# Kernel optimization log

Hardware: AMD Instinct MI355X
Metric: run time of the kernel (lower is better)

Reference implementation:

```python
import jax, jax.numpy as jnp
import numpy as np

B, S, D, H = 4, 2048, 1024, 16
DK = D // H
THETA = 10000.0


def setup_inputs() -> dict:
    key = jax.random.key(0)
    ks = jax.random.split(key, 5)
    std = (1.0 / D) ** 0.5
    return {
        "x": jax.random.normal(ks[0], (B, S, D), dtype=jnp.float32),
        "q_proj": jax.random.normal(ks[1], (D, D), dtype=jnp.float32) * std,
        "k_proj": jax.random.normal(ks[2], (D, D), dtype=jnp.float32) * std,
        "v_proj": jax.random.normal(ks[3], (D, D), dtype=jnp.float32) * std,
        "o_proj": jax.random.normal(ks[4], (D, D), dtype=jnp.float32) * std,
        "token_positions": jnp.broadcast_to(jnp.arange(S, dtype=jnp.int32), (B, S)),
    }


def _apply_rope(t, cos, sin):
    # t: (B,H,S,DK); cos/sin: (B,1,S,DK//2). Interleaved even/odd rotation.
    even = t[..., 0::2]
    odd = t[..., 1::2]
    r_even = even * cos - odd * sin
    r_odd = even * sin + odd * cos
    return jnp.stack([r_even, r_odd], axis=-1).reshape(t.shape)


def reference(x, q_proj, k_proj, v_proj, o_proj, token_positions):
    b, s, d = x.shape
    # QKV projections: weights stored (out, in) -> x @ W^T
    q = (x @ q_proj.T).reshape(b, s, H, DK).transpose(0, 2, 1, 3)  # (B,H,S,DK)
    k = (x @ k_proj.T).reshape(b, s, H, DK).transpose(0, 2, 1, 3)
    v = (x @ v_proj.T).reshape(b, s, H, DK).transpose(0, 2, 1, 3)

    # RoPE angles from token positions
    inv_freq = 1.0 / (THETA ** (jnp.arange(0, DK, 2, dtype=jnp.float32) / DK))  # (DK/2,)
    ang = token_positions.astype(jnp.float32)[..., None] * inv_freq  # (B,S,DK/2)
    cos = jnp.cos(ang)[:, None, :, :]  # (B,1,S,DK/2)
    sin = jnp.sin(ang)[:, None, :, :]
    q = _apply_rope(q, cos, sin)
    k = _apply_rope(k, cos, sin)

    # Full causal attention with explicit score matrix (faithful to source)
    scores = jnp.einsum("bhqd,bhkd->bhqk", q, k) / (DK ** 0.5)
    causal = jnp.tril(jnp.ones((s, s), dtype=bool))
    scores = jnp.where(causal, scores, -jnp.inf)
    attn = jax.nn.softmax(scores, axis=-1)
    out = jnp.einsum("bhqk,bhkd->bhqd", attn, v)  # (B,H,S,DK)
    out = out.transpose(0, 2, 1, 3).reshape(b, s, d)  # (B,S,D)
    # o_proj stored (d_out, d_model): out @ o_proj^T
    return out @ o_proj.T
```

## Files before the change

### kernel.cpp

```cpp
#include <hip/hip_runtime.h>
#include <hip/hip_bf16.h>

using bf16x8 = __attribute__((ext_vector_type(8))) short;
using f32x4  = __attribute__((ext_vector_type(4))) float;

#define MFMA_BF16(a, b, c) __builtin_amdgcn_mfma_f32_16x16x32_bf16((a), (b), (c), 0, 0, 0)

__device__ __forceinline__ unsigned short f2bf(float x) {
  union { float f; unsigned int u; } v; v.f = x;
  unsigned int r = v.u + 0x7fffu + ((v.u >> 16) & 1u);
  return (unsigned short)(r >> 16);
}

__device__ __forceinline__ unsigned int cvtpk(float a, float b) {
  __hip_bfloat162 h = __float22bfloat162_rn(make_float2(a, b));
  unsigned int u; __builtin_memcpy(&u, &h, 4); return u;
}

__device__ __forceinline__ unsigned int pack_trunc(float a, float b) {
  unsigned int ua, ub;
  __builtin_memcpy(&ua, &a, 4);
  __builtin_memcpy(&ub, &b, 4);
  return (ua >> 16) | (ub & 0xFFFF0000u);
}

__device__ __forceinline__ float fast_exp2(float x) {
#if __has_builtin(__builtin_amdgcn_exp2f)
  return __builtin_amdgcn_exp2f(x);
#else
  return exp2f(x);
#endif
}

__device__ __forceinline__ void gload16(const void* g, void* l) {
  __builtin_amdgcn_global_load_lds(
      (const __attribute__((address_space(1))) unsigned int*)g,
      (__attribute__((address_space(3))) unsigned int*)l, 16, 0, 0);
}

__device__ __forceinline__ void wait_and_barrier() {
  asm volatile("s_waitcnt vmcnt(0)" ::: "memory");
  __builtin_amdgcn_sched_barrier(0);
  __builtin_amdgcn_s_barrier();
  __builtin_amdgcn_sched_barrier(0);
}

__global__ __launch_bounds__(256) void cvt_all(const float* __restrict__ x,
                                               const float* __restrict__ qw,
                                               const float* __restrict__ kw,
                                               const float* __restrict__ vw,
                                               const float* __restrict__ ow,
                                               unsigned short* __restrict__ out) {
  const int bid = blockIdx.x;
  int seg, loc;
  if (bid < 8192) { seg = 0; loc = bid; }
  else { seg = 1 + ((bid - 8192) >> 10); loc = (bid - 8192) & 1023; }
  const float* srcs[5] = {x, qw, kw, vw, ow};
  const float* in = srcs[seg];
  const size_t obase = (seg == 0) ? 0 : ((size_t)8192 + (size_t)(seg - 1) * 1024) * 1024;
  const int i = loc * 1024 + threadIdx.x * 4;
  float4 f = *(const float4*)(in + i);
  ushort4 o;
  o.x = f2bf(f.x); o.y = f2bf(f.y); o.z = f2bf(f.z); o.w = f2bf(f.w);
  *(ushort4*)(out + obase + i) = o;
}

__global__ __launch_bounds__(256) void rope_tab_k(const int* __restrict__ pos,
                                                  float2* __restrict__ tab) {
  const int row = blockIdx.x * 8 + (threadIdx.x >> 5);
  const int i = threadIdx.x & 31;
  const float p = (float)pos[row];
  const float invf = exp2f((float)(2 * i) * (-13.287712379549609f / 64.0f));
  float sn, cs;
  sincosf(p * invf, &sn, &cs);
  tab[(size_t)row * 32 + i] = make_float2(cs, sn);
}

template <int MODE>
__global__ __launch_bounds__(256) void gemm_bt(const unsigned short* __restrict__ A,
                                               const unsigned short* __restrict__ Bw,
                                               void* __restrict__ outp,
                                               const float2* __restrict__ tab,
                                               float oscale) {
  constexpr int K = 1024;
  __shared__ __align__(16) unsigned short smem[12288];
  const int tid  = threadIdx.x;
  const int lane = tid & 63, wave = tid >> 6;
  const int wr = wave >> 1, wc = wave & 1;
  const int bid = blockIdx.x + (blockIdx.y << 3);
  const int xcd = bid & 7;
  const int t6  = bid >> 3;
  const int bn0 = (t6 & 7) * 128;
  const int bm0 = (((t6 >> 3) << 3) + xcd) * 64;
  const int lrow = lane & 15, hi = lane >> 4, lko = hi * 8;
  const int srow = tid >> 2, scol = (tid & 3) * 8;
  const unsigned short* gA = A + (size_t)(bm0 + srow) * K + scol;
  const unsigned short* gB = Bw + (size_t)(bn0 + srow) * K + scol;
  const f32x4 z = {0.f, 0.f, 0.f, 0.f};
  f32x4 acc[2][4];
#pragma unroll
  for (int i = 0; i < 2; ++i)
#pragma unroll
    for (int j = 0; j < 4; ++j) acc[i][j] = z;

  auto stage = [&](int k0, int c) {
    char* base = (char*)smem + c * 12288;
    gload16(gA + k0, base + wave * 1024);
    gload16(gB + k0, base + 4096 + wave * 1024);
    gload16(gB + k0 + (size_t)64 * K, base + 8192 + wave * 1024);
  };

  stage(0, 0);
  int cur = 0;
#pragma unroll 1
  for (int k0 = 0; k0 < K; k0 += 32) {
    wait_and_barrier();
    if (k0 + 32 < K) stage(k0 + 32, cur ^ 1);
    const int ub = cur * 6144;
    bf16x8 af[2], bfr[4];
#pragma unroll
    for (int mi = 0; mi < 2; ++mi)
      af[mi] = *(const bf16x8*)&smem[ub + (wr * 32 + mi * 16 + lrow) * 32 + lko];
#pragma unroll
    for (int ni = 0; ni < 4; ++ni)
      bfr[ni] = *(const bf16x8*)&smem[ub + 2048 + (wc * 64 + ni * 16 + lrow) * 32 + lko];
#pragma unroll
    for (int mi = 0; mi < 2; ++mi)
#pragma unroll
      for (int ni = 0; ni < 4; ++ni)
        acc[mi][ni] = MFMA_BF16(af[mi], bfr[ni], acc[mi][ni]);
    cur ^= 1;
  }

  if (MODE == 2) {
#pragma unroll
    for (int mi = 0; mi < 2; ++mi)
#pragma unroll
      for (int r = 0; r < 4; ++r) {
        const int row = bm0 + wr * 32 + mi * 16 + hi * 4 + r;
#pragma unroll
        for (int ni = 0; ni < 4; ++ni) {
          const int col = bn0 + wc * 64 + ni * 16 + lrow;
          ((float*)outp)[(size_t)row * 1024 + col] = acc[mi][ni][r];
        }
      }
    return;
  }

  const int h0 = bn0 >> 6;
  const int bb = bm0 >> 11, s0 = bm0 & 2047;
  unsigned short* dst = (unsigned short*)outp;
  __syncthreads();
  if (MODE == 0) {
#pragma unroll
    for (int mi = 0; mi < 2; ++mi)
#pragma unroll
      for (int ni = 0; ni < 4; ++ni) {
        const int col = wc * 64 + ni * 16 + lrow;
        const int d = col & 63;
#pragma unroll
        for (int r = 0; r < 4; ++r) {
          const int row = wr * 32 + mi * 16 + hi * 4 + r;
          const float2 t = tab[(size_t)(bm0 + row) * 32 + (d >> 1)];
          const float v = acc[mi][ni][r];
          const float other = __shfl_xor(v, 1);
          const float rv = (d & 1) ? (other * t.y + v * t.x) : (v * t.x - other * t.y);
          smem[row * 136 + col] = f2bf(rv * oscale);
        }
      }
    __syncthreads();
#pragma unroll
    for (int it = 0; it < 4; ++it) {
      const int c = it * 256 + tid;
      const int hl = c >> 9, rem = c & 511;
      const int sl = rem >> 3, ch = (rem & 7) * 8;
      const bf16x8 val = *(const bf16x8*)&smem[sl * 136 + hl * 64 + ch];
      *(bf16x8*)&dst[((size_t)(bb * 16 + h0 + hl) * 2048 + s0 + sl) * 64 + ch] = val;
    }
  } else {
#pragma unroll
    for (int mi = 0; mi < 2; ++mi)
#pragma unroll
      for (int ni = 0; ni < 4; ++ni) {
        const int col = wc * 64 + ni * 16 + lrow;
        ushort4 pk;
        pk.x = f2bf(acc[mi][ni][0]); pk.y = f2bf(acc[mi][ni][1]);
        pk.z = f2bf(acc[mi][ni][2]); pk.w = f2bf(acc[mi][ni][3]);
        *(ushort4*)&smem[col * 72 + wr * 32 + mi * 16 + hi * 4] = pk;
      }
    __syncthreads();
#pragma unroll
    for (int it = 0; it < 4; ++it) {
      const int c = it * 256 + tid;
      const int cl = c >> 3, sc = (c & 7) * 8;
      const bf16x8 val = *(const bf16x8*)&smem[cl * 72 + sc];
      *(bf16x8*)&dst[((size_t)(bb * 16 + h0 + (cl >> 6)) * 64 + (cl & 63)) * 2048 + s0 + sc] = val;
    }
  }
}

__global__ __launch_bounds__(256) void attn_fwd(const unsigned short* __restrict__ Q,
                                                const unsigned short* __restrict__ Kk,
                                                const unsigned short* __restrict__ Vt,
                                                unsigned short* __restrict__ O) {
  __shared__ __align__(16) unsigned short Ks[4096];
  __shared__ __align__(16) unsigned short Vs[4096];
  __shared__ __align__(16) unsigned short Plds[4][16][64];
  const int p = blockIdx.x;
  const int L = (p & 7) * 128 + (p >> 3);
  const int bh = L >> 4, pair = L & 15;
  const int tid = threadIdx.x;
  const int lane = tid & 63, wave = tid >> 6;
  const int lrow = lane & 15, hi = lane >> 4;
  const int l7 = lrow & 7;
  const unsigned short* Qb = Q + (size_t)bh * 2048 * 64;
  const unsigned short* Kb = Kk + (size_t)bh * 2048 * 64;
  const unsigned short* Vb = Vt + (size_t)bh * 64 * 2048;
  const int rowA = tid >> 3;
  const int colA = ((tid & 7) ^ (rowA & 7)) * 8;
  const int rowB = rowA + 32;
  const int colB = ((tid & 7) ^ (rowB & 7)) * 8;
  char* kBase0 = (char*)Ks + wave * 1024;
  char* kBase1 = (char*)Ks + 4096 + wave * 1024;
  char* vBase0 = (char*)Vs + wave * 1024;
  char* vBase1 = (char*)Vs + 4096 + wave * 1024;
  const int b = bh >> 4, h = bh & 15;
  const f32x4 z = {0.f, 0.f, 0.f, 0.f};
  const short one = (short)0x3F80;
  const bf16x8 ones = {one, one, one, one, one, one, one, one};

  for (int half = 0; half < 2; ++half) {
    const int qb = half ? (31 - pair) : pair;
    const int qrow = qb * 64 + wave * 16;
    const int qg = qrow + lrow;
    const bf16x8 qf0 = *(const bf16x8*)(Qb + (size_t)qg * 64 + hi * 8);
    const bf16x8 qf1 = *(const bf16x8*)(Qb + (size_t)qg * 64 + 32 + hi * 8);
    f32x4 acc[4] = {z, z, z, z};
    f32x4 acc_l = z;

    auto process = [&](int t, bool diag) {
      const int kv0 = t * 64;
      __syncthreads();
      gload16(Kb + (size_t)(kv0 + rowA) * 64 + colA, kBase0);
      gload16(Kb + (size_t)(kv0 + rowB) * 64 + colB, kBase1);
      gload16(Vb + (size_t)rowA * 2048 + kv0 + colA, vBase0);
      gload16(Vb + (size_t)rowB * 2048 + kv0 + colB, vBase1);
      __syncthreads();

      f32x4 st[4];
#pragma unroll
      for (int n = 0; n < 4; ++n) {
        const int rk = n * 16 + lrow;
        const bf16x8 kf0 = *(const bf16x8*)((char*)Ks + rk * 128 + ((hi ^ l7) * 16));
        const bf16x8 kf1 = *(const bf16x8*)((char*)Ks + rk * 128 + (((4 + hi) ^ l7) * 16));
        st[n] = MFMA_BF16(kf0, qf0, z);
        st[n] = MFMA_BF16(kf1, qf1, st[n]);
      }
      if (diag) {
#pragma unroll
        for (int n = 0; n < 4; ++n)
#pragma unroll
          for (int r = 0; r < 4; ++r)
            if (kv0 + n * 16 + hi * 4 + r > qg) st[n][r] = -1e30f;
      }
      float pe[16];
#pragma unroll
      for (int n = 0; n < 4; ++n)
#pragma unroll
        for (int r = 0; r < 4; ++r) pe[n * 4 + r] = fast_exp2(st[n][r]);
#pragma unroll
      for (int n = 0; n < 4; ++n) {
        uint2 pk;
        pk.x = pack_trunc(pe[n * 4 + 0], pe[n * 4 + 1]);
        pk.y = pack_trunc(pe[n * 4 + 2], pe[n * 4 + 3]);
        const int eo = ((((n * 2 + (hi >> 1)) ^ l7) << 3) | ((hi & 1) << 2));
        *(uint2*)&Plds[wave][lrow][eo] = pk;
      }
      const bf16x8 pf0 = *(const bf16x8*)&Plds[wave][lrow][(hi ^ l7) << 3];
      const bf16x8 pf1 = *(const bf16x8*)&Plds[wave][lrow][((4 + hi) ^ l7) << 3];
      acc_l = MFMA_BF16(ones, pf0, acc_l);
      acc_l = MFMA_BF16(ones, pf1, acc_l);
#pragma unroll
      for (int dt = 0; dt < 4; ++dt) {
        const int rv = dt * 16 + lrow;
        const bf16x8 vf0 = *(const bf16x8*)((char*)Vs + rv * 128 + ((hi ^ l7) * 16));
        const bf16x8 vf1 = *(const bf16x8*)((char*)Vs + rv * 128 + (((4 + hi) ^ l7) * 16));
        acc[dt] = MFMA_BF16(vf0, pf0, acc[dt]);
        acc[dt] = MFMA_BF16(vf1, pf1, acc[dt]);
      }
    };

#pragma unroll 1
    for (int t = 0; t < qb; ++t) process(t, false);
    process(qb, true);

    const float inv = 1.0f / acc_l[0];
#pragma unroll
    for (int dt = 0; dt < 4; ++dt) {
      uint2 ov;
      ov.x = cvtpk(acc[dt][0] * inv, acc[dt][1] * inv);
      ov.y = cvtpk(acc[dt][2] * inv, acc[dt][3] * inv);
      *(uint2*)&O[((size_t)b * 2048 + qg) * 1024 + h * 64 + dt * 16 + hi * 4] = ov;
    }
  }
}

extern "C" void kernel_launch(void* const* d_in, const int* in_sizes, int n_in,
                              void* d_out, int out_size, void* d_ws, size_t ws_size,
                              hipStream_t stream) {
  const float* x  = (const float*)d_in[0];
  const float* qw = (const float*)d_in[1];
  const float* kw = (const float*)d_in[2];
  const float* vw = (const float*)d_in[3];
  const float* ow = (const float*)d_in[4];
  const int* pos  = (const int*)d_in[5];
  float* out = (float*)d_out;

  unsigned short* xb  = (unsigned short*)d_ws;
  unsigned short* qwb = xb  + (size_t)8192 * 1024;
  unsigned short* kwb = qwb + (size_t)1024 * 1024;
  unsigned short* vwb = kwb + (size_t)1024 * 1024;
  unsigned short* owb = vwb + (size_t)1024 * 1024;
  unsigned short* Qr  = owb + (size_t)1024 * 1024;
  unsigned short* Kr  = Qr  + (size_t)8192 * 1024;
  unsigned short* Vtr = Kr  + (size_t)8192 * 1024;
  unsigned short* AO  = Vtr + (size_t)8192 * 1024;
  float2* tab = (float2*)(AO + (size_t)8192 * 1024);

  cvt_all<<<12288, 256, 0, stream>>>(x, qw, kw, vw, ow, xb);
  rope_tab_k<<<1024, 256, 0, stream>>>(pos, tab);

  constexpr float SCALE = 0.18033688011112042f;
  dim3 gg(8, 128);
  gemm_bt<0><<<gg, 256, 0, stream>>>(xb, qwb, Qr,  tab, SCALE);
  gemm_bt<0><<<gg, 256, 0, stream>>>(xb, kwb, Kr,  tab, 1.0f);
  gemm_bt<1><<<gg, 256, 0, stream>>>(xb, vwb, Vtr, nullptr, 1.0f);
  attn_fwd<<<1024, 256, 0, stream>>>(Qr, Kr, Vtr, AO);
  gemm_bt<2><<<gg, 256, 0, stream>>>(AO, owb, out, nullptr, 1.0f);
}
```

Measured before the change: 182.9 us.

## Stage 128-row KV tiles per barrier pair and raise wave priority around MFMAs

The attention loop now loads 128 keys/values per staging step (double-size LDS buffers) and runs two 64-wide compute passes per pair of barriers, with a 64-wide tail step for even diagonal blocks. This halves the number of __syncthreads and load phases per query tile. s_setprio is also raised around the MFMA sections to favour matrix issue. In exchange it doubles K/V LDS usage, which may reduce occupancy, and there is still no overlap between loading and compute.

New measurement: 181.8 us. No clear change (-0.6%).

```diff
diff --git a/kernel.cpp b/kernel.cpp
--- a/kernel.cpp
+++ b/kernel.cpp
@@ -203,8 +203,8 @@
                                                 const unsigned short* __restrict__ Kk,
                                                 const unsigned short* __restrict__ Vt,
                                                 unsigned short* __restrict__ O) {
-  __shared__ __align__(16) unsigned short Ks[4096];
-  __shared__ __align__(16) unsigned short Vs[4096];
+  __shared__ __align__(16) unsigned short Ks[8192];
+  __shared__ __align__(16) unsigned short Vs[8192];
   __shared__ __align__(16) unsigned short Plds[4][16][64];
   const int p = blockIdx.x;
   const int L = (p & 7) * 128 + (p >> 3);
@@ -216,18 +216,35 @@
   const unsigned short* Qb = Q + (size_t)bh * 2048 * 64;
   const unsigned short* Kb = Kk + (size_t)bh * 2048 * 64;
   const unsigned short* Vb = Vt + (size_t)bh * 64 * 2048;
-  const int rowA = tid >> 3;
-  const int colA = ((tid & 7) ^ (rowA & 7)) * 8;
-  const int rowB = rowA + 32;
-  const int colB = ((tid & 7) ^ (rowB & 7)) * 8;
-  char* kBase0 = (char*)Ks + wave * 1024;
-  char* kBase1 = (char*)Ks + 4096 + wave * 1024;
-  char* vBase0 = (char*)Vs + wave * 1024;
-  char* vBase1 = (char*)Vs + 4096 + wave * 1024;
+  const int rK   = tid >> 3;
+  const int colK = ((tid & 7) ^ ((tid >> 3) & 7)) * 8;
+  const int rV   = tid >> 4;
+  const int colV = ((tid & 8) | ((tid & 7) ^ ((tid >> 4) & 7))) * 8;
   const int b = bh >> 4, h = bh & 15;
   const f32x4 z = {0.f, 0.f, 0.f, 0.f};
   const short one = (short)0x3F80;
   const bf16x8 ones = {one, one, one, one, one, one, one, one};
+
+  auto stage128 = [&](int kv0) {
+#pragma unroll
+    for (int pass = 0; pass < 4; ++pass)
+      gload16(Kb + (size_t)(kv0 + rK + 32 * pass) * 64 + colK,
+              (char*)Ks + pass * 4096 + wave * 1024);
+#pragma unroll
+    for (int pass = 0; pass < 4; ++pass)
+      gload16(Vb + (size_t)(rV + 16 * pass) * 2048 + kv0 + colV,
+              (char*)Vs + pass * 4096 + wave * 1024);
+  };
+  auto stage64 = [&](int kv0) {
+#pragma unroll
+    for (int pass = 0; pass < 2; ++pass)
+      gload16(Kb + (size_t)(kv0 + rK + 32 * pass) * 64 + colK,
+              (char*)Ks + pass * 4096 + wave * 1024);
+#pragma unroll
+    for (int pass = 0; pass < 2; ++pass)
+      gload16(Vb + (size_t)(rK + 32 * pass) * 2048 + kv0 + colK,
+              (char*)Vs + pass * 4096 + wave * 1024);
+  };
 
   for (int half = 0; half < 2; ++half) {
     const int qb = half ? (31 - pair) : pair;
@@ -238,30 +255,25 @@
     f32x4 acc[4] = {z, z, z, z};
     f32x4 acc_l = z;
 
-    auto process = [&](int t, bool diag) {
-      const int kv0 = t * 64;
-      __syncthreads();
-      gload16(Kb + (size_t)(kv0 + rowA) * 64 + colA, kBase0);
-      gload16(Kb + (size_t)(kv0 + rowB) * 64 + colB, kBase1);
-      gload16(Vb + (size_t)rowA * 2048 + kv0 + colA, vBase0);
-      gload16(Vb + (size_t)rowB * 2048 + kv0 + colB, vBase1);
-      __syncthreads();
-
+    auto compute64 = [&](const char* Kbase, const char* Vbase, int vstride,
+                         int kv0g, bool diag) {
       f32x4 st[4];
+      __builtin_amdgcn_s_setprio(1);
 #pragma unroll
       for (int n = 0; n < 4; ++n) {
         const int rk = n * 16 + lrow;
-        const bf16x8 kf0 = *(const bf16x8*)((char*)Ks + rk * 128 + ((hi ^ l7) * 16));
-        const bf16x8 kf1 = *(const bf16x8*)((char*)Ks + rk * 128 + (((4 + hi) ^ l7) * 16));
+        const bf16x8 kf0 = *(const bf16x8*)(Kbase + rk * 128 + ((hi ^ l7) * 16));
+        const bf16x8 kf1 = *(const bf16x8*)(Kbase + rk * 128 + (((4 + hi) ^ l7) * 16));
         st[n] = MFMA_BF16(kf0, qf0, z);
         st[n] = MFMA_BF16(kf1, qf1, st[n]);
       }
+      __builtin_amdgcn_s_setprio(0);
       if (diag) {
 #pragma unroll
         for (int n = 0; n < 4; ++n)
 #pragma unroll
           for (int r = 0; r < 4; ++r)
-            if (kv0 + n * 16 + hi * 4 + r > qg) st[n][r] = -1e30f;
+            if (kv0g + n * 16 + hi * 4 + r > qg) st[n][r] = -1e30f;
       }
       float pe[16];
 #pragma unroll
@@ -278,21 +290,39 @@
       }
       const bf16x8 pf0 = *(const bf16x8*)&Plds[wave][lrow][(hi ^ l7) << 3];
       const bf16x8 pf1 = *(const bf16x8*)&Plds[wave][lrow][((4 + hi) ^ l7) << 3];
+      __builtin_amdgcn_s_setprio(1);
       acc_l = MFMA_BF16(ones, pf0, acc_l);
       acc_l = MFMA_BF16(ones, pf1, acc_l);
 #pragma unroll
       for (int dt = 0; dt < 4; ++dt) {
         const int rv = dt * 16 + lrow;
-        const bf16x8 vf0 = *(const bf16x8*)((char*)Vs + rv * 128 + ((hi ^ l7) * 16));
-        const bf16x8 vf1 = *(const bf16x8*)((char*)Vs + rv * 128 + (((4 + hi) ^ l7) * 16));
+        const bf16x8 vf0 = *(const bf16x8*)(Vbase + rv * vstride + ((hi ^ l7) * 16));
+        const bf16x8 vf1 = *(const bf16x8*)(Vbase + rv * vstride + (((4 + hi) ^ l7) * 16));
         acc[dt] = MFMA_BF16(vf0, pf0, acc[dt]);
         acc[dt] = MFMA_BF16(vf1, pf1, acc[dt]);
       }
+      __builtin_amdgcn_s_setprio(0);
     };
 
+    const int F = (qb + 1) >> 1;
+    const bool tail = ((qb & 1) == 0);
 #pragma unroll 1
-    for (int t = 0; t < qb; ++t) process(t, false);
-    process(qb, true);
+    for (int f = 0; f < F; ++f) {
+      const int kv0 = f * 128;
+      __syncthreads();
+      stage128(kv0);
+      __syncthreads();
+      compute64((char*)Ks, (char*)Vs, 256, kv0, false);
+      compute64((char*)Ks + 8192, (char*)Vs + 128, 256, kv0 + 64,
+                (f == F - 1) && !tail);
+    }
+    if (tail) {
+      const int kv0 = qb * 64;
+      __syncthreads();
+      stage64(kv0);
+      __syncthreads();
+      compute64((char*)Ks, (char*)Vs, 128, kv0, true);
+    }
 
     const float inv = 1.0f / acc_l[0];
 #pragma unroll
```
